# Kernel tuning notes

Hardware: AMD Instinct MI355X
Metric: run time of the kernel (lower is better)

The kernel has to match this reference:

```python
import jax, jax.numpy as jnp
import numpy as np

NUM_HEADS = 12


def setup_inputs() -> dict:
    key = jax.random.key(0)
    ks = jax.random.split(key, 7)
    n_node, n_graph, E = 1024, 4, 768
    return {
        "query": jax.random.normal(ks[0], (n_node, n_graph, E), jnp.float32),
        "attn_bias": jax.random.normal(ks[1], (n_graph * NUM_HEADS, n_node, n_node), jnp.float32),
        "node_non_padding_mask": jax.random.randint(ks[2], (n_graph, n_node), 0, 2).astype(bool),
        "W_in": jax.random.normal(ks[3], (3 * E, E), jnp.float32) * (E ** -0.5),
        "b_in": jax.random.normal(ks[4], (3 * E,), jnp.float32) * 0.02,
        "W_out": jax.random.normal(ks[5], (E, E), jnp.float32) * (E ** -0.5),
        "b_out": jax.random.normal(ks[6], (E,), jnp.float32) * 0.02,
    }


def reference(query, attn_bias, node_non_padding_mask, W_in, b_in, W_out, b_out):
    n_node, n_graph, E = query.shape
    H = NUM_HEADS
    hd = E // H
    scaling = hd ** -0.5

    # fused qkv projection, then chunk along last dim (torch .chunk(3, -1))
    qkv = query @ W_in.T + b_in                      # [N, B, 3E]
    q, k, v = jnp.split(qkv, 3, axis=-1)             # each [N, B, E]

    def to_bh(x):
        # [N, B, E] -> [N, B*H, hd] -> [B*H, N, hd]
        return x.reshape(n_node, n_graph * H, hd).transpose(1, 0, 2)

    q = to_bh(q) * scaling
    k = to_bh(k)
    v = to_bh(v)

    attn_weights = jnp.einsum('bnd,bmd->bnm', q, k) + attn_bias   # [B*H, N, N]
    attn_probs = jax.nn.softmax(attn_weights, axis=-1)            # dropout=0 (eval)
    attn = jnp.einsum('bnm,bmd->bnd', attn_probs, v)              # [B*H, N, hd]
    attn = attn.transpose(1, 0, 2).reshape(n_node, n_graph, E)

    out = attn @ W_out.T + b_out                                   # [N, B, E]
    mask = node_non_padding_mask.T[:, :, None]                     # [N, B, 1]
    return jnp.where(mask, out, 0.0)
```

## Files before the change

### kernel.cpp

```cpp
#include <hip/hip_runtime.h>
#include <hip/hip_bf16.h>

#define NNODE 1024
#define NGRAPH 4
#define EDIM 768
#define NH 12
#define HD 64
#define NBH 48
#define MTOK 4096
#define QKVN 2304

typedef __attribute__((ext_vector_type(8))) short bf16x8;
typedef __attribute__((ext_vector_type(4))) short bf16x4;
typedef __attribute__((ext_vector_type(4))) float f32x4;

static __device__ __forceinline__ short f2s(float f) {
    union { float f; unsigned u; } c; c.f = f;
    unsigned r = (c.u + 0x7FFFu + ((c.u >> 16) & 1u)) >> 16;
    return (short)r;
}

__global__ __launch_bounds__(256) void cvt_bf16(
    const float* __restrict__ in, short* __restrict__ out, int n)
{
    const int i = (blockIdx.x * 256 + threadIdx.x) * 8;
    float4 a = *(const float4*)(in + i);
    float4 b = *(const float4*)(in + i + 4);
    bf16x8 v;
    v[0] = f2s(a.x); v[1] = f2s(a.y); v[2] = f2s(a.z); v[3] = f2s(a.w);
    v[4] = f2s(b.x); v[5] = f2s(b.y); v[6] = f2s(b.z); v[7] = f2s(b.w);
    *(bf16x8*)(out + i) = v;
}

__global__ __launch_bounds__(256) void gemm_bt(
    const short* __restrict__ A,
    const short* __restrict__ B,
    const float* __restrict__ bias,
    void* __restrict__ Cv,
    int M, int N, int K, int mode, const int* __restrict__ mask)
{
    const int LDK = 72;
    __shared__ __align__(16) short As[64 * LDK];
    __shared__ __align__(16) short Bs[64 * LDK];

    const int m0 = blockIdx.x * 64;
    const int n0 = blockIdx.y * 64;
    const int t = threadIdx.x;
    const int w = t >> 6, l = t & 63;
    const int wm = (w & 1) * 32, wn = (w >> 1) * 32;
    const int ldr = t >> 2;
    const int ldc = (t & 3) * 16;

    f32x4 acc[2][2];
    #pragma unroll
    for (int i = 0; i < 2; i++)
        #pragma unroll
        for (int j = 0; j < 2; j++)
            acc[i][j] = (f32x4){0.f, 0.f, 0.f, 0.f};

    const int lr = l & 15;
    const int lk = (l >> 4) * 8;

    for (int kt = 0; kt < K; kt += 64) {
        const short* ap = A + (size_t)(m0 + ldr) * K + kt + ldc;
        const short* bp = B + (size_t)(n0 + ldr) * K + kt + ldc;
        uint4 a0 = *(const uint4*)(ap);
        uint4 a1 = *(const uint4*)(ap + 8);
        uint4 b0 = *(const uint4*)(bp);
        uint4 b1 = *(const uint4*)(bp + 8);
        *(uint4*)(&As[ldr * LDK + ldc]) = a0;
        *(uint4*)(&As[ldr * LDK + ldc + 8]) = a1;
        *(uint4*)(&Bs[ldr * LDK + ldc]) = b0;
        *(uint4*)(&Bs[ldr * LDK + ldc + 8]) = b1;
        __syncthreads();

        #pragma unroll
        for (int ks = 0; ks < 2; ks++) {
            bf16x8 af0 = *(const bf16x8*)(&As[(wm + lr) * LDK + ks * 32 + lk]);
            bf16x8 af1 = *(const bf16x8*)(&As[(wm + 16 + lr) * LDK + ks * 32 + lk]);
            bf16x8 bf0 = *(const bf16x8*)(&Bs[(wn + lr) * LDK + ks * 32 + lk]);
            bf16x8 bf1 = *(const bf16x8*)(&Bs[(wn + 16 + lr) * LDK + ks * 32 + lk]);
            acc[0][0] = __builtin_amdgcn_mfma_f32_16x16x32_bf16(af0, bf0, acc[0][0], 0, 0, 0);
            acc[0][1] = __builtin_amdgcn_mfma_f32_16x16x32_bf16(af0, bf1, acc[0][1], 0, 0, 0);
            acc[1][0] = __builtin_amdgcn_mfma_f32_16x16x32_bf16(af1, bf0, acc[1][0], 0, 0, 0);
            acc[1][1] = __builtin_amdgcn_mfma_f32_16x16x32_bf16(af1, bf1, acc[1][1], 0, 0, 0);
        }
        __syncthreads();
    }

    const int lq = l >> 4;
    short* Cb = (short*)Cv;
    float* Cf = (float*)Cv;
    #pragma unroll
    for (int i = 0; i < 2; i++) {
        #pragma unroll
        for (int j = 0; j < 2; j++) {
            const int col = n0 + wn + j * 16 + lr;
            const float bcol = bias[col];
            #pragma unroll
            for (int r = 0; r < 4; r++) {
                const int row = m0 + wm + i * 16 + lq * 4 + r;
                float v = acc[i][j][r] + bcol;
                if (mode == 0) {
                    if (col < EDIM) v *= 0.125f;
                    Cb[(size_t)row * N + col] = f2s(v);
                } else {
                    const int nn = row >> 2, bb = row & 3;
                    if (mask[bb * NNODE + nn] == 0) v = 0.f;
                    Cf[(size_t)row * N + col] = v;
                }
            }
        }
    }
}

#define FLDK 72
#define FLDP 72
__global__ __launch_bounds__(256) void flash_attn(
    const short* __restrict__ qkv,
    const float* __restrict__ attn_bias,
    short* __restrict__ attn)
{
    __shared__ __align__(16) short Ks[64 * FLDK];
    __shared__ __align__(16) short Vt[64 * FLDK];
    __shared__ __align__(16) short Ps[4][16 * FLDP];

    const int bh = blockIdx.y;
    const int b = bh / NH, h = bh - b * NH;
    const int q0 = blockIdx.x * 64;
    const int t = threadIdx.x;
    const int w = t >> 6, l = t & 63;
    const int c = l & 15, g = l >> 4;

    const int qrow = q0 + w * 16 + c;
    const short* qptr = qkv + (size_t)(qrow * NGRAPH + b) * QKVN + h * HD + g * 8;
    bf16x8 qa0 = *(const bf16x8*)(qptr);
    bf16x8 qa1 = *(const bf16x8*)(qptr + 32);

    const int skrow = t >> 3;
    const int scol8 = (t & 7) * 8;
    const int sxor = scol8 & 0x38;

    float m_st[4], l_st[4];
    f32x4 o[4];
    #pragma unroll
    for (int r = 0; r < 4; r++) { m_st[r] = -3e38f; l_st[r] = 0.f; }
    #pragma unroll
    for (int ct = 0; ct < 4; ct++) o[ct] = (f32x4){0.f, 0.f, 0.f, 0.f};

    const float* bp_base = attn_bias + (size_t)bh * NNODE * NNODE
                         + (size_t)(q0 + w * 16) * NNODE;
    float bpre[16];
    #pragma unroll
    for (int ct = 0; ct < 4; ct++)
        #pragma unroll
        for (int r = 0; r < 4; r++)
            bpre[ct * 4 + r] = bp_base[(size_t)(g * 4 + r) * NNODE + ct * 16 + c];

    for (int k0 = 0; k0 < NNODE; k0 += 64) {
        __syncthreads();
        #pragma unroll
        for (int p = 0; p < 2; p++) {
            const int kr = skrow + p * 32;
            const short* kvp = qkv + (size_t)((k0 + kr) * NGRAPH + b) * QKVN + h * HD + scol8;
            bf16x8 kk = *(const bf16x8*)(kvp + EDIM);
            bf16x8 vv = *(const bf16x8*)(kvp + 2 * EDIM);
            *(bf16x8*)&Ks[kr * FLDK + scol8] = kk;
            const int kks = kr ^ sxor;
            #pragma unroll
            for (int j = 0; j < 8; j++)
                Vt[(scol8 + j) * FLDK + kks] = vv[j];
        }
        __syncthreads();

        f32x4 s[4];
        #pragma unroll
        for (int ct = 0; ct < 4; ct++)
            #pragma unroll
            for (int r = 0; r < 4; r++)
                s[ct][r] = bpre[ct * 4 + r];

        const int knext = (k0 + 64) & (NNODE - 1);
        #pragma unroll
        for (int ct = 0; ct < 4; ct++)
            #pragma unroll
            for (int r = 0; r < 4; r++)
                bpre[ct * 4 + r] = bp_base[(size_t)(g * 4 + r) * NNODE + knext + ct * 16 + c];

        #pragma unroll
        for (int ct = 0; ct < 4; ct++) {
            bf16x8 kb0 = *(const bf16x8*)&Ks[(ct * 16 + c) * FLDK + g * 8];
            bf16x8 kb1 = *(const bf16x8*)&Ks[(ct * 16 + c) * FLDK + 32 + g * 8];
            s[ct] = __builtin_amdgcn_mfma_f32_16x16x32_bf16(qa0, kb0, s[ct], 0, 0, 0);
            s[ct] = __builtin_amdgcn_mfma_f32_16x16x32_bf16(qa1, kb1, s[ct], 0, 0, 0);
        }

        float mn[4], alpha[4];
        #pragma unroll
        for (int r = 0; r < 4; r++) {
            float mx = fmaxf(fmaxf(s[0][r], s[1][r]), fmaxf(s[2][r], s[3][r]));
            #pragma unroll
            for (int off = 1; off < 16; off <<= 1)
                mx = fmaxf(mx, __shfl_xor(mx, off));
            mn[r] = fmaxf(m_st[r], mx);
            alpha[r] = __expf(m_st[r] - mn[r]);
            m_st[r] = mn[r];
        }
        float rs[4] = {0.f, 0.f, 0.f, 0.f};
        #pragma unroll
        for (int ct = 0; ct < 4; ct++) {
            #pragma unroll
            for (int r = 0; r < 4; r++) {
                float pv = __expf(s[ct][r] - mn[r]);
                s[ct][r] = pv;
                rs[r] += pv;
            }
        }
        #pragma unroll
        for (int r = 0; r < 4; r++) {
            #pragma unroll
            for (int off = 1; off < 16; off <<= 1)
                rs[r] += __shfl_xor(rs[r], off);
            l_st[r] = alpha[r] * l_st[r] + rs[r];
        }
        #pragma unroll
        for (int ct = 0; ct < 4; ct++)
            #pragma unroll
            for (int r = 0; r < 4; r++)
                o[ct][r] *= alpha[r];

        short* ps = &Ps[w][0];
        #pragma unroll
        for (int ct = 0; ct < 4; ct++)
            #pragma unroll
            for (int r = 0; r < 4; r++)
                ps[(g * 4 + r) * FLDP + ct * 16 + c] = f2s(s[ct][r]);

        bf16x8 pa0 = *(const bf16x8*)&ps[c * FLDP + g * 8];
        bf16x8 pa1 = *(const bf16x8*)&ps[c * FLDP + 32 + g * 8];
        #pragma unroll
        for (int ct = 0; ct < 4; ct++) {
            const int d = ct * 16 + c;
            const int x = d & 0x38;
            bf16x8 vb0 = *(const bf16x8*)&Vt[d * FLDK + ((g * 8) ^ x)];
            bf16x8 vb1 = *(const bf16x8*)&Vt[d * FLDK + ((32 + g * 8) ^ x)];
            o[ct] = __builtin_amdgcn_mfma_f32_16x16x32_bf16(pa0, vb0, o[ct], 0, 0, 0);
            o[ct] = __builtin_amdgcn_mfma_f32_16x16x32_bf16(pa1, vb1, o[ct], 0, 0, 0);
        }
    }

    float inv[4];
    #pragma unroll
    for (int r = 0; r < 4; r++) inv[r] = 1.f / l_st[r];
    #pragma unroll
    for (int ct = 0; ct < 4; ct++) {
        #pragma unroll
        for (int r = 0; r < 4; r++) {
            const int n = q0 + w * 16 + g * 4 + r;
            attn[(size_t)(n * NGRAPH + b) * EDIM + h * HD + ct * 16 + c] =
                f2s(o[ct][r] * inv[r]);
        }
    }
}

extern "C" void kernel_launch(void* const* d_in, const int* in_sizes, int n_in,
                              void* d_out, int out_size, void* d_ws, size_t ws_size,
                              hipStream_t stream) {
    const float* query     = (const float*)d_in[0];
    const float* attn_bias = (const float*)d_in[1];
    const int*   mask      = (const int*)d_in[2];
    const float* W_in      = (const float*)d_in[3];
    const float* b_in      = (const float*)d_in[4];
    const float* W_out     = (const float*)d_in[5];
    const float* b_out     = (const float*)d_in[6];
    float* out = (float*)d_out;

    short* qkv     = (short*)d_ws;
    short* attn    = qkv + (size_t)MTOK * QKVN;
    short* q_bf    = attn + (size_t)MTOK * EDIM;
    short* win_bf  = q_bf + (size_t)MTOK * EDIM;
    short* wout_bf = win_bf + (size_t)QKVN * EDIM;

    cvt_bf16<<<(MTOK * EDIM) / 2048, 256, 0, stream>>>(query, q_bf, MTOK * EDIM);
    cvt_bf16<<<(QKVN * EDIM) / 2048, 256, 0, stream>>>(W_in, win_bf, QKVN * EDIM);
    cvt_bf16<<<(EDIM * EDIM) / 2048, 256, 0, stream>>>(W_out, wout_bf, EDIM * EDIM);

    {
        dim3 grid(MTOK / 64, QKVN / 64);
        gemm_bt<<<grid, 256, 0, stream>>>(q_bf, win_bf, b_in, qkv,
                                          MTOK, QKVN, EDIM, 0, nullptr);
    }
    {
        dim3 grid(NNODE / 64, NBH);
        flash_attn<<<grid, 256, 0, stream>>>(qkv, attn_bias, attn);
    }
    {
        dim3 grid(MTOK / 64, EDIM / 64);
        gemm_bt<<<grid, 256, 0, stream>>>(attn, wout_bf, b_out, out,
                                          MTOK, EDIM, EDIM, 1, mask);
    }
}
```

Baseline: 364.9 us.

## Enlarge GEMM tiles to 128x128 with direct global-to-LDS loads; prefetch K/V in attention

The projection GEMM now uses 128x128 block tiles, with each wave computing a 64x64 subtile via 4x4 MFMA accumulators. Tiles are staged with global_load_lds, which writes directly into unpadded shared memory instead of going through registers. The aim is more data reuse per load and less VGPR traffic. The flash attention kernel also register-prefetches the next K/V tile so global latency overlaps with compute. Risks include LDS bank conflicts from the unpadded layout, fewer blocks for the output GEMM (192 blocks), and higher register pressure.

```diff
diff --git a/kernel.cpp b/kernel.cpp
--- a/kernel.cpp
+++ b/kernel.cpp
@@ -11,13 +11,19 @@
 #define QKVN 2304
 
 typedef __attribute__((ext_vector_type(8))) short bf16x8;
-typedef __attribute__((ext_vector_type(4))) short bf16x4;
 typedef __attribute__((ext_vector_type(4))) float f32x4;
 
 static __device__ __forceinline__ short f2s(float f) {
     union { float f; unsigned u; } c; c.f = f;
     unsigned r = (c.u + 0x7FFFu + ((c.u >> 16) & 1u)) >> 16;
     return (short)r;
+}
+
+static __device__ __forceinline__ void gload_lds16(const short* g, short* l) {
+    __builtin_amdgcn_global_load_lds(
+        (const __attribute__((address_space(1))) unsigned int*)g,
+        (__attribute__((address_space(3))) unsigned int*)l,
+        16, 0, 0);
 }
 
 __global__ __launch_bounds__(256) void cvt_bf16(
@@ -39,76 +45,93 @@
     void* __restrict__ Cv,
     int M, int N, int K, int mode, const int* __restrict__ mask)
 {
-    const int LDK = 72;
-    __shared__ __align__(16) short As[64 * LDK];
-    __shared__ __align__(16) short Bs[64 * LDK];
-
-    const int m0 = blockIdx.x * 64;
-    const int n0 = blockIdx.y * 64;
+    __shared__ __align__(16) short As[128 * 64];
+    __shared__ __align__(16) short Bs[128 * 64];
+
+    const int m0 = blockIdx.x * 128;
+    const int n0 = blockIdx.y * 128;
     const int t = threadIdx.x;
     const int w = t >> 6, l = t & 63;
-    const int wm = (w & 1) * 32, wn = (w >> 1) * 32;
-    const int ldr = t >> 2;
-    const int ldc = (t & 3) * 16;
-
-    f32x4 acc[2][2];
-    #pragma unroll
-    for (int i = 0; i < 2; i++)
-        #pragma unroll
-        for (int j = 0; j < 2; j++)
+    const int wm = (w & 1) * 64, wn = (w >> 1) * 64;
+    const int c = l & 15, g = l >> 4;
+
+    const int srow = l >> 3;
+    const int scol = (l & 7) * 8;
+
+    f32x4 acc[4][4];
+    #pragma unroll
+    for (int i = 0; i < 4; i++)
+        #pragma unroll
+        for (int j = 0; j < 4; j++)
             acc[i][j] = (f32x4){0.f, 0.f, 0.f, 0.f};
 
-    const int lr = l & 15;
-    const int lk = (l >> 4) * 8;
-
     for (int kt = 0; kt < K; kt += 64) {
-        const short* ap = A + (size_t)(m0 + ldr) * K + kt + ldc;
-        const short* bp = B + (size_t)(n0 + ldr) * K + kt + ldc;
-        uint4 a0 = *(const uint4*)(ap);
-        uint4 a1 = *(const uint4*)(ap + 8);
-        uint4 b0 = *(const uint4*)(bp);
-        uint4 b1 = *(const uint4*)(bp + 8);
-        *(uint4*)(&As[ldr * LDK + ldc]) = a0;
-        *(uint4*)(&As[ldr * LDK + ldc + 8]) = a1;
-        *(uint4*)(&Bs[ldr * LDK + ldc]) = b0;
-        *(uint4*)(&Bs[ldr * LDK + ldc + 8]) = b1;
         __syncthreads();
+        #pragma unroll
+        for (int j = 0; j < 4; j++) {
+            const int rr = (w * 4 + j) * 8 + srow;
+            gload_lds16(A + (size_t)(m0 + rr) * K + kt + scol, &As[(w * 4 + j) * 512]);
+            gload_lds16(B + (size_t)(n0 + rr) * K + kt + scol, &Bs[(w * 4 + j) * 512]);
+        }
+        __syncthreads();
 
         #pragma unroll
         for (int ks = 0; ks < 2; ks++) {
-            bf16x8 af0 = *(const bf16x8*)(&As[(wm + lr) * LDK + ks * 32 + lk]);
-            bf16x8 af1 = *(const bf16x8*)(&As[(wm + 16 + lr) * LDK + ks * 32 + lk]);
-            bf16x8 bf0 = *(const bf16x8*)(&Bs[(wn + lr) * LDK + ks * 32 + lk]);
-            bf16x8 bf1 = *(const bf16x8*)(&Bs[(wn + 16 + lr) * LDK + ks * 32 + lk]);
-            acc[0][0] = __builtin_amdgcn_mfma_f32_16x16x32_bf16(af0, bf0, acc[0][0], 0, 0, 0);
-            acc[0][1] = __builtin_amdgcn_mfma_f32_16x16x32_bf16(af0, bf1, acc[0][1], 0, 0, 0);
-            acc[1][0] = __builtin_amdgcn_mfma_f32_16x16x32_bf16(af1, bf0, acc[1][0], 0, 0, 0);
-            acc[1][1] = __builtin_amdgcn_mfma_f32_16x16x32_bf16(af1, bf1, acc[1][1], 0, 0, 0);
-        }
-        __syncthreads();
-    }
-
-    const int lq = l >> 4;
-    short* Cb = (short*)Cv;
-    float* Cf = (float*)Cv;
-    #pragma unroll
-    for (int i = 0; i < 2; i++) {
-        #pragma unroll
-        for (int j = 0; j < 2; j++) {
-            const int col = n0 + wn + j * 16 + lr;
-            const float bcol = bias[col];
+            bf16x8 af[4], bf[4];
+            #pragma unroll
+            for (int i = 0; i < 4; i++)
+                af[i] = *(const bf16x8*)&As[(wm + i * 16 + c) * 64 + ks * 32 + g * 8];
+            #pragma unroll
+            for (int j = 0; j < 4; j++)
+                bf[j] = *(const bf16x8*)&Bs[(wn + j * 16 + c) * 64 + ks * 32 + g * 8];
+            #pragma unroll
+            for (int i = 0; i < 4; i++)
+                #pragma unroll
+                for (int j = 0; j < 4; j++)
+                    acc[i][j] = __builtin_amdgcn_mfma_f32_16x16x32_bf16(af[i], bf[j], acc[i][j], 0, 0, 0);
+        }
+    }
+
+    float bcol[4];
+    #pragma unroll
+    for (int j = 0; j < 4; j++) bcol[j] = bias[n0 + wn + j * 16 + c];
+
+    if (mode == 0) {
+        short* Cb = (short*)Cv;
+        #pragma unroll
+        for (int i = 0; i < 4; i++) {
             #pragma unroll
             for (int r = 0; r < 4; r++) {
-                const int row = m0 + wm + i * 16 + lq * 4 + r;
-                float v = acc[i][j][r] + bcol;
-                if (mode == 0) {
+                const int row = m0 + wm + i * 16 + g * 4 + r;
+                short* crow = Cb + (size_t)row * N + n0 + wn + c;
+                #pragma unroll
+                for (int j = 0; j < 4; j++) {
+                    const int col = n0 + wn + j * 16 + c;
+                    float v = acc[i][j][r] + bcol[j];
                     if (col < EDIM) v *= 0.125f;
-                    Cb[(size_t)row * N + col] = f2s(v);
-                } else {
-                    const int nn = row >> 2, bb = row & 3;
-                    if (mask[bb * NNODE + nn] == 0) v = 0.f;
-                    Cf[(size_t)row * N + col] = v;
+                    crow[j * 16] = f2s(v);
                 }
+            }
+        }
+    } else {
+        float* Cf = (float*)Cv;
+        float mfac[4][4];
+        #pragma unroll
+        for (int i = 0; i < 4; i++)
+            #pragma unroll
+            for (int r = 0; r < 4; r++) {
+                const int row = m0 + wm + i * 16 + g * 4 + r;
+                mfac[i][r] = mask[(row & 3) * NNODE + (row >> 2)] ? 1.f : 0.f;
+            }
+        #pragma unroll
+        for (int i = 0; i < 4; i++) {
+            #pragma unroll
+            for (int r = 0; r < 4; r++) {
+                const int row = m0 + wm + i * 16 + g * 4 + r;
+                float* crow = Cf + (size_t)row * N + n0 + wn + c;
+                #pragma unroll
+                for (int j = 0; j < 4; j++)
+                    crow[j * 16] = (acc[i][j][r] + bcol[j]) * mfac[i][r];
             }
         }
     }
@@ -157,21 +180,34 @@
         for (int r = 0; r < 4; r++)
             bpre[ct * 4 + r] = bp_base[(size_t)(g * 4 + r) * NNODE + ct * 16 + c];
 
+    bf16x8 kk[2], vv[2];
+    #pragma unroll
+    for (int p = 0; p < 2; p++) {
+        const short* kvp = qkv + (size_t)((skrow + p * 32) * NGRAPH + b) * QKVN + h * HD + scol8;
+        kk[p] = *(const bf16x8*)(kvp + EDIM);
+        vv[p] = *(const bf16x8*)(kvp + 2 * EDIM);
+    }
+
     for (int k0 = 0; k0 < NNODE; k0 += 64) {
         __syncthreads();
         #pragma unroll
         for (int p = 0; p < 2; p++) {
             const int kr = skrow + p * 32;
-            const short* kvp = qkv + (size_t)((k0 + kr) * NGRAPH + b) * QKVN + h * HD + scol8;
-            bf16x8 kk = *(const bf16x8*)(kvp + EDIM);
-            bf16x8 vv = *(const bf16x8*)(kvp + 2 * EDIM);
-            *(bf16x8*)&Ks[kr * FLDK + scol8] = kk;
+            *(bf16x8*)&Ks[kr * FLDK + scol8] = kk[p];
             const int kks = kr ^ sxor;
             #pragma unroll
             for (int j = 0; j < 8; j++)
-                Vt[(scol8 + j) * FLDK + kks] = vv[j];
+                Vt[(scol8 + j) * FLDK + kks] = vv[p][j];
         }
         __syncthreads();
+
+        const int kn = (k0 + 64) & (NNODE - 1);
+        #pragma unroll
+        for (int p = 0; p < 2; p++) {
+            const short* kvp = qkv + (size_t)((kn + skrow + p * 32) * NGRAPH + b) * QKVN + h * HD + scol8;
+            kk[p] = *(const bf16x8*)(kvp + EDIM);
+            vv[p] = *(const bf16x8*)(kvp + 2 * EDIM);
+        }
 
         f32x4 s[4];
         #pragma unroll
@@ -286,7 +322,7 @@
     cvt_bf16<<<(EDIM * EDIM) / 2048, 256, 0, stream>>>(W_out, wout_bf, EDIM * EDIM);
 
     {
-        dim3 grid(MTOK / 64, QKVN / 64);
+        dim3 grid(MTOK / 128, QKVN / 128);
         gemm_bt<<<grid, 256, 0, stream>>>(q_bf, win_bf, b_in, qkv,
                                           MTOK, QKVN, EDIM, 0, nullptr);
     }
@@ -295,7 +331,7 @@
         flash_attn<<<grid, 256, 0, stream>>>(qkv, attn_bias, attn);
     }
     {
-        dim3 grid(MTOK / 64, EDIM / 64);
+        dim3 grid(MTOK / 128, EDIM / 128);
         gemm_bt<<<grid, 256, 0, stream>>>(attn, wout_bf, b_out, out,
                                           MTOK, EDIM, EDIM, 1, mask);
     }
```

After: 391.9 us. 1.07x slower.
